# Optimization experiments

Measured on AMD Instinct MI355X. Metric: run time of the kernel, lower is better.

The kernel has to match this reference:

```python
import jax, jax.numpy as jnp
import numpy as np

N_HEADS = 16
D_HEAD = 64
IGNORE = -100000.0


def setup_inputs() -> dict:
    key = jax.random.key(0)
    ks = jax.random.split(key, 5)
    B, S, D = 2, 2048, 1024
    return {
        "residual": jax.random.normal(ks[0], (B, S, D), dtype=jnp.float32),
        "q": jax.random.normal(ks[1], (B, S, D), dtype=jnp.float32),
        "k": jax.random.normal(ks[2], (B, S, D), dtype=jnp.float32),
        "v": jax.random.normal(ks[3], (B, S, D), dtype=jnp.float32),
        "W_O": jax.random.normal(ks[4], (N_HEADS, D_HEAD, D), dtype=jnp.float32) * 0.02,
        "b_O": jnp.zeros((D,), dtype=jnp.float32),
    }


def reference(residual, q, k, v, W_O, b_O):
    B, S, _ = q.shape
    attn_scale = np.sqrt(D_HEAD).astype(np.float32)  # use_attn_scale=True
    # split heads: [..., pos, (h d)] -> [..., pos, h, d]
    qh = q.reshape(B, S, N_HEADS, D_HEAD)
    kh = k.reshape(B, S, N_HEADS, D_HEAD)
    vh = v.reshape(B, S, N_HEADS, D_HEAD)
    # scores: [..., head, query_pos, key_pos]
    scores = jnp.einsum("bqhd,bkhd->bhqk", qh, kh) / attn_scale
    causal = jnp.tril(jnp.ones((S, S), dtype=bool))
    scores = jnp.where(causal, scores, jnp.float32(IGNORE))
    pattern = jax.nn.softmax(scores, axis=-1)
    # weighted sum of values: [..., query_pos, head, d_head]
    z = jnp.einsum("bkhd,bhqk->bqhd", vh, pattern)
    out = jnp.einsum("bqhd,hdm->bqm", z, W_O) + b_O
    return (residual, out)
```

## Files before the change

kernel.cpp:

```cpp
#include <hip/hip_runtime.h>

#define B_ 2
#define S_ 2048
#define D_ 1024
#define H_ 16
#define DH_ 64
#define NP_ 2048

typedef short v8s __attribute__((ext_vector_type(8)));
typedef float v4f __attribute__((ext_vector_type(4)));
typedef float v16f __attribute__((ext_vector_type(16)));
typedef unsigned int v2u __attribute__((ext_vector_type(2)));
typedef unsigned int v4u __attribute__((ext_vector_type(4)));
typedef unsigned int uint32;

__device__ inline short f2bf(float f) {
  unsigned u = __float_as_uint(f);
  u = (u + 0x7FFFu + ((u >> 16) & 1u)) >> 16;
  return (short)u;
}

__device__ inline unsigned pk_bf16(float lo, float hi) {
  unsigned r;
  asm("v_cvt_pk_bf16_f32 %0, %1, %2" : "=v"(r) : "v"(lo), "v"(hi));
  return r;
}

__device__ inline void gll16(const void* g, void* l) {
  __builtin_amdgcn_global_load_lds(
      (const __attribute__((address_space(1))) void*)g,
      (__attribute__((address_space(3))) void*)l, 16, 0, 0);
}

__global__ __launch_bounds__(256) void cvt_all_kernel(
    const float* __restrict__ k, short* __restrict__ kb,
    const float* __restrict__ v, short* __restrict__ vt,
    const float* __restrict__ w, short* __restrict__ wt) {
  __shared__ short t[64][64 + 8];
  int bid = blockIdx.x;
  int tid = threadIdx.x;
  if (bid < 2048) {
    int i = bid * 256 + tid;
    float4 a = ((const float4*)k)[2 * i];
    float4 b = ((const float4*)k)[2 * i + 1];
    v8s o;
    o[0] = f2bf(a.x); o[1] = f2bf(a.y); o[2] = f2bf(a.z); o[3] = f2bf(a.w);
    o[4] = f2bf(b.x); o[5] = f2bf(b.y); o[6] = f2bf(b.z); o[7] = f2bf(b.w);
    ((v8s*)kb)[i] = o;
    return;
  }
  int r = tid >> 2, c16 = (tid & 3) * 16;
  if (bid < 3072) {
    int id = bid - 2048;
    int st = id & 31;
    int bh = id >> 5;
    int b = bh >> 4, h = bh & 15;
    const float* vp = v + ((size_t)(b * S_ + st * 64 + r)) * D_ + h * DH_ + c16;
    for (int i = 0; i < 16; i += 4) {
      float4 a = *(const float4*)(vp + i);
      t[r][c16 + i + 0] = f2bf(a.x);
      t[r][c16 + i + 1] = f2bf(a.y);
      t[r][c16 + i + 2] = f2bf(a.z);
      t[r][c16 + i + 3] = f2bf(a.w);
    }
    __syncthreads();
    short* op = vt + ((size_t)((b * H_ + h) * DH_ + r)) * S_ + st * 64 + c16;
    v8s o0, o1;
    for (int j = 0; j < 8; ++j) { o0[j] = t[c16 + j][r]; o1[j] = t[c16 + 8 + j][r]; }
    *(v8s*)op = o0;
    *(v8s*)(op + 8) = o1;
  } else {
    int id = bid - 3072;
    int tk = id & 15, tm = id >> 4;
    const float* wp = w + (size_t)(tk * 64 + r) * D_ + tm * 64 + c16;
    for (int i = 0; i < 16; i += 4) {
      float4 a = *(const float4*)(wp + i);
      t[r][c16 + i + 0] = f2bf(a.x);
      t[r][c16 + i + 1] = f2bf(a.y);
      t[r][c16 + i + 2] = f2bf(a.z);
      t[r][c16 + i + 3] = f2bf(a.w);
    }
    __syncthreads();
    short* op = wt + (size_t)(tm * 64 + r) * D_ + tk * 64 + c16;
    v8s o0, o1;
    for (int j = 0; j < 8; ++j) { o0[j] = t[c16 + j][r]; o1[j] = t[c16 + 8 + j][r]; }
    *(v8s*)op = o0;
    *(v8s*)(op + 8) = o1;
  }
}

template <int SPLITS>
__global__ __launch_bounds__(128, 4) void attn_kernel(
    const float* __restrict__ q, const short* __restrict__ kbf,
    const short* __restrict__ vtb, uint32* __restrict__ Opart,
    float* __restrict__ Lsum, const float* __restrict__ residual,
    float* __restrict__ res_out) {
  constexpr int SHIFT = (SPLITS == 2 ? 6 : 5);
  int bid = blockIdx.x;
  int bh = bid & 31;
  int sp = (SPLITS == 2) ? ((bid >> 5) & 1) : 0;
  int qt = 31 - (int)(bid >> SHIFT);
  int b = bh >> 4, h = bh & 15;

  int nt = qt + 1;
  int hs = (nt + 1) >> 1;
  int t0 = (SPLITS == 2 && sp == 1) ? hs : 0;
  int t1 = (SPLITS == 2 && sp == 0) ? hs - 1 : qt;

  int tid = threadIdx.x;
  int wave = tid >> 6, lane = tid & 63;
  int l31 = lane & 31, h32 = lane >> 5;

  __shared__ short Klds[64][64];
  __shared__ short Vlds[64][64];

  const int qrow0 = qt * 64 + wave * 32;
  const int lr8 = lane >> 3;
  const int scol = ((lane & 7) ^ lr8) << 3;

  const short* pk_ = kbf + (size_t)b * S_ * D_ + h * DH_ +
                     (size_t)(t0 * 64 + wave * 8 + lr8) * D_ + scol;
  const short* pv_ = vtb + (size_t)(b * H_ + h) * DH_ * S_ +
                     (size_t)(wave * 8 + lr8) * S_ + t0 * 64 + scol;

  v8s qf[4];
  {
    const float* qp = q + (size_t)(b * S_ + qrow0 + l31) * D_ + h * DH_ + h32 * 8;
    const float sc = 0.125f * 1.44269504f;
#pragma unroll
    for (int d4 = 0; d4 < 4; ++d4) {
      float4 x = *(const float4*)(qp + d4 * 16);
      float4 y = *(const float4*)(qp + d4 * 16 + 4);
      v8s tq;
      tq[0] = f2bf(x.x * sc); tq[1] = f2bf(x.y * sc);
      tq[2] = f2bf(x.z * sc); tq[3] = f2bf(x.w * sc);
      tq[4] = f2bf(y.x * sc); tq[5] = f2bf(y.y * sc);
      tq[6] = f2bf(y.z * sc); tq[7] = f2bf(y.w * sc);
      qf[d4] = tq;
    }
  }

  v16f O0, O1;
#pragma unroll
  for (int r = 0; r < 16; ++r) { O0[r] = 0.f; O1[r] = 0.f; }
  float L = 0.f;
  const int swz = (l31 & 7) << 3;

  for (int s = t0; s <= t1; ++s) {
#pragma unroll
    for (int i = 0; i < 4; ++i)
      gll16(pk_ + (size_t)(i * 16) * D_, &Klds[i * 16 + wave * 8][0]);
#pragma unroll
    for (int i = 0; i < 4; ++i)
      gll16(pv_ + (size_t)(i * 16) * S_, &Vlds[i * 16 + wave * 8][0]);
    pk_ += (size_t)64 * D_;
    pv_ += 64;
    asm volatile("s_waitcnt vmcnt(0)" ::: "memory");
    __builtin_amdgcn_sched_barrier(0);
    __builtin_amdgcn_s_barrier();
    __builtin_amdgcn_sched_barrier(0);

    int kb = s * 64;
    bool skip1 = (kb >= qrow0);
    bool msk = (kb + 63 > qrow0);

    __builtin_amdgcn_s_setprio(1);
    v16f S0, S1;
#pragma unroll
    for (int r = 0; r < 16; ++r) { S0[r] = 0.f; S1[r] = 0.f; }
#pragma unroll
    for (int d4 = 0; d4 < 4; ++d4) {
      v8s kf = *(const v8s*)&Klds[l31][(((d4 << 1) | h32) << 3) ^ swz];
      S0 = __builtin_amdgcn_mfma_f32_32x32x16_bf16(kf, qf[d4], S0, 0, 0, 0);
    }
    if (!skip1) {
#pragma unroll
      for (int d4 = 0; d4 < 4; ++d4) {
        v8s kf = *(const v8s*)&Klds[32 + l31][(((d4 << 1) | h32) << 3) ^ swz];
        S1 = __builtin_amdgcn_mfma_f32_32x32x16_bf16(kf, qf[d4], S1, 0, 0, 0);
      }
    }
    __builtin_amdgcn_s_setprio(0);

    int qg = qrow0 + l31;
    if (msk) {
#pragma unroll
      for (int r = 0; r < 16; ++r) {
        int kl = kb + (r & 3) + 8 * (r >> 2) + 4 * h32;
        if (kl > qg) S0[r] = -1e30f;
      }
      if (!skip1) {
#pragma unroll
        for (int r = 0; r < 16; ++r) {
          int kl = kb + 32 + (r & 3) + 8 * (r >> 2) + 4 * h32;
          if (kl > qg) S1[r] = -1e30f;
        }
      }
    }

    float rs = 0.f;
    unsigned pw0[8], pw1[8];
#pragma unroll
    for (int r = 0; r < 16; ++r) {
      S0[r] = __builtin_amdgcn_exp2f(S0[r]);
      rs += S0[r];
    }
#pragma unroll
    for (int w = 0; w < 8; ++w) pw0[w] = pk_bf16(S0[2 * w], S0[2 * w + 1]);
    if (!skip1) {
#pragma unroll
      for (int r = 0; r < 16; ++r) {
        S1[r] = __builtin_amdgcn_exp2f(S1[r]);
        rs += S1[r];
      }
#pragma unroll
      for (int w = 0; w < 8; ++w) pw1[w] = pk_bf16(S1[2 * w], S1[2 * w + 1]);
    }
    rs += __shfl_xor(rs, 32);
    L += rs;

    __builtin_amdgcn_s_setprio(1);
#pragma unroll
    for (int ks = 0; ks < 2; ++ks) {
      v2u a = __builtin_amdgcn_permlane32_swap(pw0[ks * 4 + 0], pw0[ks * 4 + 2], false, false);
      v2u c = __builtin_amdgcn_permlane32_swap(pw0[ks * 4 + 1], pw0[ks * 4 + 3], false, false);
      v4u fw; fw.x = a.x; fw.y = c.x; fw.z = a.y; fw.w = c.y;
      v8s pb = __builtin_bit_cast(v8s, fw);
      v8s vf0 = *(const v8s*)&Vlds[l31][(((ks << 1) | h32) << 3) ^ swz];
      O0 = __builtin_amdgcn_mfma_f32_32x32x16_bf16(vf0, pb, O0, 0, 0, 0);
      v8s vf1 = *(const v8s*)&Vlds[32 + l31][(((ks << 1) | h32) << 3) ^ swz];
      O1 = __builtin_amdgcn_mfma_f32_32x32x16_bf16(vf1, pb, O1, 0, 0, 0);
    }
    if (!skip1) {
#pragma unroll
      for (int ks = 0; ks < 2; ++ks) {
        v2u a = __builtin_amdgcn_permlane32_swap(pw1[ks * 4 + 0], pw1[ks * 4 + 2], false, false);
        v2u c = __builtin_amdgcn_permlane32_swap(pw1[ks * 4 + 1], pw1[ks * 4 + 3], false, false);
        v4u fw; fw.x = a.x; fw.y = c.x; fw.z = a.y; fw.w = c.y;
        v8s pb = __builtin_bit_cast(v8s, fw);
        v8s vf0 = *(const v8s*)&Vlds[l31][((((ks + 2) << 1) | h32) << 3) ^ swz];
        O0 = __builtin_amdgcn_mfma_f32_32x32x16_bf16(vf0, pb, O0, 0, 0, 0);
        v8s vf1 = *(const v8s*)&Vlds[32 + l31][((((ks + 2) << 1) | h32) << 3) ^ swz];
        O1 = __builtin_amdgcn_mfma_f32_32x32x16_bf16(vf1, pb, O1, 0, 0, 0);
      }
    }
    __builtin_amdgcn_s_setprio(0);

    __builtin_amdgcn_sched_barrier(0);
    __builtin_amdgcn_s_barrier();
    __builtin_amdgcn_sched_barrier(0);
  }

  int p = bh * 64 + qt * 2 + wave;
  uint32* Op = Opart + ((size_t)(sp * NP_ + p)) * 1024;
#pragma unroll
  for (int w = 0; w < 8; ++w) {
    int dpair = 4 * (w >> 1) + (w & 1) + 2 * h32;
    Op[dpair * 32 + l31] = pk_bf16(O0[2 * w], O0[2 * w + 1]);
    Op[(16 + dpair) * 32 + l31] = pk_bf16(O1[2 * w], O1[2 * w + 1]);
  }
  if (h32 == 0) Lsum[(size_t)(sp * NP_ + p) * 32 + l31] = L;

  {
    constexpr int F4 = (SPLITS == 2) ? 4 : 8;
    const float4* rs_ = (const float4*)residual;
    float4* rd_ = (float4*)res_out;
    size_t base = (size_t)bid * (128 * F4) + tid;
#pragma unroll
    for (int j = 0; j < F4; ++j) rd_[base + j * 128] = rs_[base + j * 128];
  }
}

template <int SPLITS>
__global__ __launch_bounds__(128) void merge_kernel(
    const uint32* __restrict__ Opart, const float* __restrict__ Lsum,
    short* __restrict__ z) {
  int p = blockIdx.x;
  int tid = threadIdx.x;
  int qq = tid & 31, g = tid >> 5;

  float Lt = Lsum[(size_t)p * 32 + qq];
  if constexpr (SPLITS == 2) Lt += Lsum[((size_t)NP_ + p) * 32 + qq];
  float f = 1.f / Lt;

  __shared__ uint32 T[32][33];
#pragma unroll
  for (int j = 0; j < 8; ++j) {
    int dp = g * 8 + j;
    uint32 u0 = Opart[(size_t)p * 1024 + dp * 32 + qq];
    float lo = __uint_as_float(u0 << 16);
    float hi = __uint_as_float(u0 & 0xFFFF0000u);
    if constexpr (SPLITS == 2) {
      uint32 u1 = Opart[((size_t)NP_ + p) * 1024 + dp * 32 + qq];
      lo += __uint_as_float(u1 << 16);
      hi += __uint_as_float(u1 & 0xFFFF0000u);
    }
    T[qq][dp] = pk_bf16(lo * f, hi * f);
  }
  __syncthreads();
  int q2 = tid >> 2, c = (tid & 3) * 8;
  int srow = (p & 63) * 32 + q2;
  int b = p >> 10, h = (p >> 6) & 15;
  uint32* zp = (uint32*)z + ((size_t)(b * S_ + srow)) * (D_ / 2) + h * 32 + c;
#pragma unroll
  for (int j = 0; j < 8; ++j) zp[j] = T[q2][c + j];
}

__global__ __launch_bounds__(256) void proj_kernel(
    const short* __restrict__ z, const short* __restrict__ wt,
    const float* __restrict__ bias, float* __restrict__ out) {
  int bid = blockIdx.x;
  int bm = bid & 31, bn = bid >> 5;
  int tid = threadIdx.x;
  int wave = tid >> 6, lane = tid & 63, lh = lane >> 4, ll = lane & 15;
  int wr = wave >> 1, wc = wave & 1;

  __shared__ short Al[2][128][64];
  __shared__ short Bl[2][128][64];

  const int r8 = lane >> 3;
  const int scol = ((lane & 7) ^ r8) << 3;

  v4f acc[4][4];
#pragma unroll
  for (int m = 0; m < 4; ++m)
#pragma unroll
    for (int n = 0; n < 4; ++n) acc[m][n] = (v4f){0.f, 0.f, 0.f, 0.f};

  auto stage = [&](int kb, int bbuf) {
#pragma unroll
    for (int i = 0; i < 4; ++i) {
      int c = wave * 4 + i;
      gll16(z + (size_t)(bm * 128 + c * 8 + r8) * D_ + kb + scol, &Al[bbuf][c * 8][0]);
    }
#pragma unroll
    for (int i = 0; i < 4; ++i) {
      int c = wave * 4 + i;
      gll16(wt + (size_t)(bn * 128 + c * 8 + r8) * D_ + kb + scol, &Bl[bbuf][c * 8][0]);
    }
  };

  stage(0, 0);
  __syncthreads();

  for (int kt = 0; kt < D_ / 64; ++kt) {
    int bbuf = kt & 1;
    if (kt + 1 < D_ / 64) stage((kt + 1) * 64, bbuf ^ 1);
    v8s af[4][2], bf[4][2];
#pragma unroll
    for (int m = 0; m < 4; ++m) {
      int row = wr * 64 + m * 16 + ll;
#pragma unroll
      for (int c = 0; c < 2; ++c)
        af[m][c] = *(const v8s*)&Al[bbuf][row][(((c << 2) | lh) ^ (ll & 7)) << 3];
    }
#pragma unroll
    for (int n = 0; n < 4; ++n) {
      int row = wc * 64 + n * 16 + ll;
#pragma unroll
      for (int c = 0; c < 2; ++c)
        bf[n][c] = *(const v8s*)&Bl[bbuf][row][(((c << 2) | lh) ^ (ll & 7)) << 3];
    }
#pragma unroll
    for (int m = 0; m < 4; ++m)
#pragma unroll
      for (int n = 0; n < 4; ++n)
#pragma unroll
        for (int c = 0; c < 2; ++c)
          acc[m][n] = __builtin_amdgcn_mfma_f32_16x16x32_bf16(af[m][c], bf[n][c], acc[m][n], 0, 0, 0);
    __syncthreads();
  }

#pragma unroll
  for (int m = 0; m < 4; ++m) {
    int gr = bm * 128 + wr * 64 + m * 16 + lh * 4;
#pragma unroll
    for (int n = 0; n < 4; ++n) {
      int gc = bn * 128 + wc * 64 + n * 16 + ll;
      float bo = bias[gc];
#pragma unroll
      for (int r = 0; r < 4; ++r)
        out[(size_t)(gr + r) * D_ + gc] = acc[m][n][r] + bo;
    }
  }
}

extern "C" void kernel_launch(void* const* d_in, const int* in_sizes, int n_in,
                              void* d_out, int out_size, void* d_ws, size_t ws_size,
                              hipStream_t stream) {
  const float* residual = (const float*)d_in[0];
  const float* q = (const float*)d_in[1];
  const float* k = (const float*)d_in[2];
  const float* v = (const float*)d_in[3];
  const float* W = (const float*)d_in[4];
  const float* bO = (const float*)d_in[5];
  float* out = (float*)d_out;

  const size_t half = (size_t)B_ * S_ * D_;
  char* ws = (char*)d_ws;
  short* kbf = (short*)ws;
  short* vtb = kbf + half;
  short* wtb = vtb + half;
  char* pbase = (char*)(wtb + (size_t)D_ * D_);
  const size_t opart_b = (size_t)NP_ * 1024 * 4;
  const size_t l_b = (size_t)NP_ * 32 * 4;
  const size_t base_b = (size_t)pbase - (size_t)ws;
  short* z = kbf;

  cvt_all_kernel<<<3328, 256, 0, stream>>>(k, kbf, v, vtb, W, wtb);

  if (ws_size >= base_b + 2 * (opart_b + l_b)) {
    uint32* Opart = (uint32*)pbase;
    float* Lsum = (float*)(pbase + 2 * opart_b);
    attn_kernel<2><<<2048, 128, 0, stream>>>(q, kbf, vtb, Opart, Lsum, residual, out);
    merge_kernel<2><<<NP_, 128, 0, stream>>>(Opart, Lsum, z);
  } else {
    uint32* Opart = (uint32*)pbase;
    float* Lsum = (float*)(pbase + opart_b);
    attn_kernel<1><<<1024, 128, 0, stream>>>(q, kbf, vtb, Opart, Lsum, residual, out);
    merge_kernel<1><<<NP_, 128, 0, stream>>>(Opart, Lsum, z);
  }
  proj_kernel<<<256, 256, 0, stream>>>(z, wtb, bO, out + half);
}
```

Measured before the change: 74.11 us.

## Fuse split-KV merge into output projection GEMM A-tile loading

Removes the separate merge kernel. The projection GEMM now reads the partial attention outputs and row sums directly, combines the splits, normalizes, converts to bf16 and writes the A tile into shared memory with swizzle. This removes one kernel launch and the z round trip through global memory. In exchange, A loading goes through registers with strided 4-byte global loads instead of async direct-to-LDS loads, which adds register pressure and ALU work inside the GEMM loop.

```diff
diff --git a/kernel.cpp b/kernel.cpp
--- a/kernel.cpp
+++ b/kernel.cpp
@@ -272,43 +272,10 @@
 }
 
 template <int SPLITS>
-__global__ __launch_bounds__(128) void merge_kernel(
+__global__ __launch_bounds__(256) void proj_kernel(
     const uint32* __restrict__ Opart, const float* __restrict__ Lsum,
-    short* __restrict__ z) {
-  int p = blockIdx.x;
-  int tid = threadIdx.x;
-  int qq = tid & 31, g = tid >> 5;
-
-  float Lt = Lsum[(size_t)p * 32 + qq];
-  if constexpr (SPLITS == 2) Lt += Lsum[((size_t)NP_ + p) * 32 + qq];
-  float f = 1.f / Lt;
-
-  __shared__ uint32 T[32][33];
-#pragma unroll
-  for (int j = 0; j < 8; ++j) {
-    int dp = g * 8 + j;
-    uint32 u0 = Opart[(size_t)p * 1024 + dp * 32 + qq];
-    float lo = __uint_as_float(u0 << 16);
-    float hi = __uint_as_float(u0 & 0xFFFF0000u);
-    if constexpr (SPLITS == 2) {
-      uint32 u1 = Opart[((size_t)NP_ + p) * 1024 + dp * 32 + qq];
-      lo += __uint_as_float(u1 << 16);
-      hi += __uint_as_float(u1 & 0xFFFF0000u);
-    }
-    T[qq][dp] = pk_bf16(lo * f, hi * f);
-  }
-  __syncthreads();
-  int q2 = tid >> 2, c = (tid & 3) * 8;
-  int srow = (p & 63) * 32 + q2;
-  int b = p >> 10, h = (p >> 6) & 15;
-  uint32* zp = (uint32*)z + ((size_t)(b * S_ + srow)) * (D_ / 2) + h * 32 + c;
-#pragma unroll
-  for (int j = 0; j < 8; ++j) zp[j] = T[q2][c + j];
-}
-
-__global__ __launch_bounds__(256) void proj_kernel(
-    const short* __restrict__ z, const short* __restrict__ wt,
-    const float* __restrict__ bias, float* __restrict__ out) {
+    const short* __restrict__ wt, const float* __restrict__ bias,
+    float* __restrict__ out) {
   int bid = blockIdx.x;
   int bm = bid & 31, bn = bid >> 5;
   int tid = threadIdx.x;
@@ -321,45 +288,87 @@
   const int r8 = lane >> 3;
   const int scol = ((lane & 7) ^ r8) << 3;
 
+  const int ss = tid >> 6;
+  const int sq = lane & 31;
+  const int sg = lane >> 5;
+  const int arow = ss * 32 + sq;
+  const int ax7 = arow & 7;
+  const int ab = bm >> 4;
+  const int j0 = (bm & 15) * 4;
+
   v4f acc[4][4];
 #pragma unroll
   for (int m = 0; m < 4; ++m)
 #pragma unroll
     for (int n = 0; n < 4; ++n) acc[m][n] = (v4f){0.f, 0.f, 0.f, 0.f};
 
-  auto stage = [&](int kb, int bbuf) {
+  uint32 a0[16], a1[16];
+  float f;
+
+  auto loadA = [&](int kt) {
+    size_t p = ((size_t)(ab * 16 + kt)) * 64 + j0 + ss;
+    const uint32* src = Opart + p * 1024 + (sg * 16) * 32 + sq;
+#pragma unroll
+    for (int j = 0; j < 16; ++j) a0[j] = src[j * 32];
+    if constexpr (SPLITS == 2) {
+      const uint32* src1 = src + (size_t)NP_ * 1024;
+#pragma unroll
+      for (int j = 0; j < 16; ++j) a1[j] = src1[j * 32];
+    }
+    float Lt = Lsum[p * 32 + sq];
+    if constexpr (SPLITS == 2) Lt += Lsum[((size_t)NP_ + p) * 32 + sq];
+    f = 1.f / Lt;
+  };
+
+  auto writeA = [&](int buf) {
+#pragma unroll
+    for (int j = 0; j < 16; ++j) {
+      int dp = sg * 16 + j;
+      float lo = __uint_as_float(a0[j] << 16);
+      float hi = __uint_as_float(a0[j] & 0xFFFF0000u);
+      if constexpr (SPLITS == 2) {
+        lo += __uint_as_float(a1[j] << 16);
+        hi += __uint_as_float(a1[j] & 0xFFFF0000u);
+      }
+      uint32 w = pk_bf16(lo * f, hi * f);
+      int g = dp >> 2;
+      *(uint32*)&Al[buf][arow][((g ^ ax7) << 3) + ((dp & 3) << 1)] = w;
+    }
+  };
+
+  auto stageB = [&](int kb, int buf) {
 #pragma unroll
     for (int i = 0; i < 4; ++i) {
       int c = wave * 4 + i;
-      gll16(z + (size_t)(bm * 128 + c * 8 + r8) * D_ + kb + scol, &Al[bbuf][c * 8][0]);
-    }
-#pragma unroll
-    for (int i = 0; i < 4; ++i) {
-      int c = wave * 4 + i;
-      gll16(wt + (size_t)(bn * 128 + c * 8 + r8) * D_ + kb + scol, &Bl[bbuf][c * 8][0]);
+      gll16(wt + (size_t)(bn * 128 + c * 8 + r8) * D_ + kb + scol, &Bl[buf][c * 8][0]);
     }
   };
 
-  stage(0, 0);
+  loadA(0);
+  stageB(0, 0);
+  writeA(0);
   __syncthreads();
 
-  for (int kt = 0; kt < D_ / 64; ++kt) {
-    int bbuf = kt & 1;
-    if (kt + 1 < D_ / 64) stage((kt + 1) * 64, bbuf ^ 1);
+  for (int kt = 0; kt < 16; ++kt) {
+    int buf = kt & 1;
+    if (kt + 1 < 16) {
+      loadA(kt + 1);
+      stageB((kt + 1) * 64, buf ^ 1);
+    }
     v8s af[4][2], bf[4][2];
 #pragma unroll
     for (int m = 0; m < 4; ++m) {
       int row = wr * 64 + m * 16 + ll;
 #pragma unroll
       for (int c = 0; c < 2; ++c)
-        af[m][c] = *(const v8s*)&Al[bbuf][row][(((c << 2) | lh) ^ (ll & 7)) << 3];
+        af[m][c] = *(const v8s*)&Al[buf][row][(((c << 2) | lh) ^ (ll & 7)) << 3];
     }
 #pragma unroll
     for (int n = 0; n < 4; ++n) {
       int row = wc * 64 + n * 16 + ll;
 #pragma unroll
       for (int c = 0; c < 2; ++c)
-        bf[n][c] = *(const v8s*)&Bl[bbuf][row][(((c << 2) | lh) ^ (ll & 7)) << 3];
+        bf[n][c] = *(const v8s*)&Bl[buf][row][(((c << 2) | lh) ^ (ll & 7)) << 3];
     }
 #pragma unroll
     for (int m = 0; m < 4; ++m)
@@ -368,6 +377,7 @@
 #pragma unroll
         for (int c = 0; c < 2; ++c)
           acc[m][n] = __builtin_amdgcn_mfma_f32_16x16x32_bf16(af[m][c], bf[n][c], acc[m][n], 0, 0, 0);
+    if (kt + 1 < 16) writeA(buf ^ 1);
     __syncthreads();
   }
 
@@ -405,7 +415,6 @@
   const size_t opart_b = (size_t)NP_ * 1024 * 4;
   const size_t l_b = (size_t)NP_ * 32 * 4;
   const size_t base_b = (size_t)pbase - (size_t)ws;
-  short* z = kbf;
 
   cvt_all_kernel<<<3328, 256, 0, stream>>>(k, kbf, v, vtb, W, wtb);
 
@@ -413,12 +422,11 @@
     uint32* Opart = (uint32*)pbase;
     float* Lsum = (float*)(pbase + 2 * opart_b);
     attn_kernel<2><<<2048, 128, 0, stream>>>(q, kbf, vtb, Opart, Lsum, residual, out);
-    merge_kernel<2><<<NP_, 128, 0, stream>>>(Opart, Lsum, z);
+    proj_kernel<2><<<256, 256, 0, stream>>>(Opart, Lsum, wtb, bO, out + half);
   } else {
     uint32* Opart = (uint32*)pbase;
     float* Lsum = (float*)(pbase + opart_b);
     attn_kernel<1><<<1024, 128, 0, stream>>>(q, kbf, vtb, Opart, Lsum, residual, out);
-    merge_kernel<1><<<NP_, 128, 0, stream>>>(Opart, Lsum, z);
-  }
-  proj_kernel<<<256, 256, 0, stream>>>(z, wtb, bO, out + half);
-}
+    proj_kernel<1><<<256, 256, 0, stream>>>(Opart, Lsum, wtb, bO, out + half);
+  }
+}
```

After: 80.74 us. 1.09x slower.
